# Performance work log

Hardware: AMD Instinct MI355X
Metric: run time of the kernel (lower is better)

## Reference

```python
import jax, jax.numpy as jnp
import numpy as np

N_NODES = 100000
N_HIDDEN = 128
N_EDGES = 625000
EPS = 1e-12  # F.normalize default eps


def setup_inputs() -> dict:
    key = jax.random.key(0)
    k1, k2, k3 = jax.random.split(key, 3)
    emb = jax.random.normal(k1, (N_NODES, N_HIDDEN), dtype=jnp.float32)
    edge_src = jax.random.randint(k2, (N_EDGES,), 0, N_NODES, dtype=jnp.int64)
    edge_dst = jax.random.randint(k3, (N_EDGES,), 0, N_NODES, dtype=jnp.int64)
    d = jnp.ones((N_HIDDEN,), dtype=jnp.float32)
    scale = jnp.ones((1,), dtype=jnp.float32)
    return {"emb": emb, "edge_src": edge_src, "edge_dst": edge_dst, "d": d, "scale": scale}


def reference(emb, edge_src, edge_dst, d, scale):
    # L2 normalize rows (torch F.normalize: x / max(||x||, eps))
    norm = jnp.linalg.norm(emb, axis=1, keepdims=True)
    e = emb / jnp.maximum(norm, EPS)            # [N, H]
    ew = e * d                                  # diag scale, [N, H]
    # edge-wise u_dot_v: sum over feature dim of ew[src] * e[dst]
    z = jnp.sum(ew[edge_src] * e[edge_dst], axis=1, keepdims=True)  # [E, 1]
    return z * scale
```

## Files before the change

kernel.cpp:

```cpp
#include <hip/hip_runtime.h>

#define NORM_EPS 1e-12f

#if defined(__has_builtin) && __has_builtin(__builtin_amdgcn_sdot4)
__device__ __forceinline__ int sdot4(unsigned a, unsigned b, int c) {
    return __builtin_amdgcn_sdot4((int)a, (int)b, c, false);
}
#else
__device__ __forceinline__ int sdot4(unsigned a, unsigned b, int c) {
    #pragma unroll
    for (int i = 0; i < 4; ++i)
        c += (int)(signed char)(a >> (8 * i)) * (int)(signed char)(b >> (8 * i));
    return c;
}
#endif

__global__ void build_tables_kernel(const float* __restrict__ emb,
                                    const float* __restrict__ dvec,
                                    unsigned short* __restrict__ tblW,
                                    unsigned short* __restrict__ tblE,
                                    float* __restrict__ sclW,
                                    float* __restrict__ sclE,
                                    int n_nodes) {
    int row  = (blockIdx.x * blockDim.x + threadIdx.x) >> 6;
    int lane = threadIdx.x & 63;
    if (row >= n_nodes) return;

    const float2* p = (const float2*)(emb + (size_t)row * 128);
    float2 v = p[lane];
    float s = v.x * v.x + v.y * v.y;
    #pragma unroll
    for (int off = 32; off > 0; off >>= 1)
        s += __shfl_xor(s, off);
    float inv = 1.0f / fmaxf(sqrtf(s), NORM_EPS);

    float e0 = v.x * inv, e1 = v.y * inv;
    float2 d2 = ((const float2*)dvec)[lane];
    float w0 = e0 * d2.x, w1 = e1 * d2.y;

    float mW = fmaxf(fabsf(w0), fabsf(w1));
    float mE = fmaxf(fabsf(e0), fabsf(e1));
    #pragma unroll
    for (int off = 32; off > 0; off >>= 1) {
        mW = fmaxf(mW, __shfl_xor(mW, off));
        mE = fmaxf(mE, __shfl_xor(mE, off));
    }

    float qW = (mW > 0.f) ? 127.0f / mW : 0.f;
    float qE = (mE > 0.f) ? 127.0f / mE : 0.f;
    int qw0 = __float2int_rn(w0 * qW), qw1 = __float2int_rn(w1 * qW);
    int qe0 = __float2int_rn(e0 * qE), qe1 = __float2int_rn(e1 * qE);

    tblW[(size_t)row * 64 + lane] =
        (unsigned short)((qw0 & 0xFF) | ((qw1 & 0xFF) << 8));
    tblE[(size_t)row * 64 + lane] =
        (unsigned short)((qe0 & 0xFF) | ((qe1 & 0xFF) << 8));
    if (lane == 0) {
        sclW[row] = mW * (1.0f / 127.0f);
        sclE[row] = mE * (1.0f / 127.0f);
    }
}

__global__ void edge_dot_i8_kernel(const uint4* __restrict__ tW,
                                   const uint4* __restrict__ tE,
                                   const float* __restrict__ sW,
                                   const float* __restrict__ sE,
                                   const int* __restrict__ esrc,
                                   const int* __restrict__ edst,
                                   const float* __restrict__ scale,
                                   float* __restrict__ out,
                                   int n_edges) {
    int g    = (blockIdx.x * blockDim.x + threadIdx.x) >> 3;
    int lane = threadIdx.x & 7;
    int e0 = g * 2, e1 = e0 + 1;
    if (e0 >= n_edges) return;
    bool has1 = e1 < n_edges;

    int s0 = esrc[e0], t0 = edst[e0];
    int s1 = has1 ? esrc[e1] : s0;
    int t1 = has1 ? edst[e1] : t0;

    uint4 a0 = tW[(size_t)s0 * 8 + lane];
    uint4 b0 = tE[(size_t)t0 * 8 + lane];
    uint4 a1 = tW[(size_t)s1 * 8 + lane];
    uint4 b1 = tE[(size_t)t1 * 8 + lane];

    float ss0 = sW[s0] * sE[t0];
    float ss1 = sW[s1] * sE[t1];

    int i0 = 0, i1 = 0;
    i0 = sdot4(a0.x, b0.x, i0); i0 = sdot4(a0.y, b0.y, i0);
    i0 = sdot4(a0.z, b0.z, i0); i0 = sdot4(a0.w, b0.w, i0);
    i1 = sdot4(a1.x, b1.x, i1); i1 = sdot4(a1.y, b1.y, i1);
    i1 = sdot4(a1.z, b1.z, i1); i1 = sdot4(a1.w, b1.w, i1);

    #pragma unroll
    for (int off = 4; off > 0; off >>= 1) {
        i0 += __shfl_xor(i0, off);
        i1 += __shfl_xor(i1, off);
    }

    if (lane == 0) {
        float sc = scale[0];
        out[e0] = (float)i0 * ss0 * sc;
        if (has1) out[e1] = (float)i1 * ss1 * sc;
    }
}

extern "C" void kernel_launch(void* const* d_in, const int* in_sizes, int n_in,
                              void* d_out, int out_size, void* d_ws, size_t ws_size,
                              hipStream_t stream) {
    const float* emb   = (const float*)d_in[0];
    const int*   esrc  = (const int*)d_in[1];
    const int*   edst  = (const int*)d_in[2];
    const float* dvec  = (const float*)d_in[3];
    const float* scale = (const float*)d_in[4];
    float*       out   = (float*)d_out;

    int n_nodes = in_sizes[0] / 128;
    int n_edges = in_sizes[1];

    char* base = (char*)d_ws;
    size_t tbl_bytes = (size_t)n_nodes * 128;
    unsigned short* tblW = (unsigned short*)base;
    unsigned short* tblE = (unsigned short*)(base + tbl_bytes);
    float*          sclW = (float*)(base + 2 * tbl_bytes);
    float*          sclE = (float*)(base + 2 * tbl_bytes + (size_t)n_nodes * 4);

    {
        int blocks = (n_nodes + 3) / 4;
        build_tables_kernel<<<blocks, 256, 0, stream>>>(
            emb, dvec, tblW, tblE, sclW, sclE, n_nodes);
    }
    {
        int n_groups = (n_edges + 1) / 2;
        long long threads = (long long)n_groups * 8;
        int blocks = (int)((threads + 255) / 256);
        edge_dot_i8_kernel<<<blocks, 256, 0, stream>>>(
            (const uint4*)tblW, (const uint4*)tblE, sclW, sclE,
            esrc, edst, scale, out, n_edges);
    }
}
```

Baseline: 131.5 us.

## Fold diagonal scale symmetrically via sqrt(|d|) to share one int8 table

Splits the diagonal weight as sqrt(|d|) on both sides of the dot product, so a single quantized table and a single scale array serve both source and destination gathers when d has no negative entries. A second sign-flipped table is written only when d contains negatives, chosen at runtime through a flag. This halves the table footprint in the common case, which should improve L2/MALL hit rates for the random gathers and cut build-kernel writes. The cost is an extra flag read per thread and slightly different quantization error.

```diff
diff --git a/kernel.cpp b/kernel.cpp
--- a/kernel.cpp
+++ b/kernel.cpp
@@ -17,10 +17,10 @@
 
 __global__ void build_tables_kernel(const float* __restrict__ emb,
                                     const float* __restrict__ dvec,
+                                    unsigned short* __restrict__ tblE,
                                     unsigned short* __restrict__ tblW,
-                                    unsigned short* __restrict__ tblE,
-                                    float* __restrict__ sclW,
-                                    float* __restrict__ sclE,
+                                    float* __restrict__ scl,
+                                    int* __restrict__ flag,
                                     int n_nodes) {
     int row  = (blockIdx.x * blockDim.x + threadIdx.x) >> 6;
     int lane = threadIdx.x & 63;
@@ -34,37 +34,40 @@
         s += __shfl_xor(s, off);
     float inv = 1.0f / fmaxf(sqrtf(s), NORM_EPS);
 
-    float e0 = v.x * inv, e1 = v.y * inv;
     float2 d2 = ((const float2*)dvec)[lane];
-    float w0 = e0 * d2.x, w1 = e1 * d2.y;
+    bool neg_lane = (d2.x < 0.0f) || (d2.y < 0.0f);
+    int has_neg = (__ballot(neg_lane) != 0ull) ? 1 : 0;
 
-    float mW = fmaxf(fabsf(w0), fabsf(w1));
-    float mE = fmaxf(fabsf(e0), fabsf(e1));
+    float r0 = sqrtf(fabsf(d2.x)), r1 = sqrtf(fabsf(d2.y));
+    float e0 = v.x * inv * r0, e1 = v.y * inv * r1;
+
+    float m = fmaxf(fabsf(e0), fabsf(e1));
     #pragma unroll
-    for (int off = 32; off > 0; off >>= 1) {
-        mW = fmaxf(mW, __shfl_xor(mW, off));
-        mE = fmaxf(mE, __shfl_xor(mE, off));
-    }
+    for (int off = 32; off > 0; off >>= 1)
+        m = fmaxf(m, __shfl_xor(m, off));
 
-    float qW = (mW > 0.f) ? 127.0f / mW : 0.f;
-    float qE = (mE > 0.f) ? 127.0f / mE : 0.f;
-    int qw0 = __float2int_rn(w0 * qW), qw1 = __float2int_rn(w1 * qW);
-    int qe0 = __float2int_rn(e0 * qE), qe1 = __float2int_rn(e1 * qE);
-
-    tblW[(size_t)row * 64 + lane] =
-        (unsigned short)((qw0 & 0xFF) | ((qw1 & 0xFF) << 8));
+    float q = (m > 0.f) ? 127.0f / m : 0.f;
+    int qe0 = __float2int_rn(e0 * q), qe1 = __float2int_rn(e1 * q);
     tblE[(size_t)row * 64 + lane] =
         (unsigned short)((qe0 & 0xFF) | ((qe1 & 0xFF) << 8));
+
+    if (has_neg) {
+        float w0 = (d2.x < 0.0f) ? -e0 : e0;
+        float w1 = (d2.y < 0.0f) ? -e1 : e1;
+        int qw0 = __float2int_rn(w0 * q), qw1 = __float2int_rn(w1 * q);
+        tblW[(size_t)row * 64 + lane] =
+            (unsigned short)((qw0 & 0xFF) | ((qw1 & 0xFF) << 8));
+    }
     if (lane == 0) {
-        sclW[row] = mW * (1.0f / 127.0f);
-        sclE[row] = mE * (1.0f / 127.0f);
+        scl[row] = m * (1.0f / 127.0f);
+        if (row == 0) flag[0] = has_neg;
     }
 }
 
-__global__ void edge_dot_i8_kernel(const uint4* __restrict__ tW,
-                                   const uint4* __restrict__ tE,
-                                   const float* __restrict__ sW,
-                                   const float* __restrict__ sE,
+__global__ void edge_dot_i8_kernel(const uint4* __restrict__ tE,
+                                   const uint4* __restrict__ tW,
+                                   const float* __restrict__ scl,
+                                   const int* __restrict__ flag,
                                    const int* __restrict__ esrc,
                                    const int* __restrict__ edst,
                                    const float* __restrict__ scale,
@@ -76,17 +79,19 @@
     if (e0 >= n_edges) return;
     bool has1 = e1 < n_edges;
 
+    const uint4* tS = (flag[0] != 0) ? tW : tE;
+
     int s0 = esrc[e0], t0 = edst[e0];
     int s1 = has1 ? esrc[e1] : s0;
     int t1 = has1 ? edst[e1] : t0;
 
-    uint4 a0 = tW[(size_t)s0 * 8 + lane];
+    uint4 a0 = tS[(size_t)s0 * 8 + lane];
     uint4 b0 = tE[(size_t)t0 * 8 + lane];
-    uint4 a1 = tW[(size_t)s1 * 8 + lane];
+    uint4 a1 = tS[(size_t)s1 * 8 + lane];
     uint4 b1 = tE[(size_t)t1 * 8 + lane];
 
-    float ss0 = sW[s0] * sE[t0];
-    float ss1 = sW[s1] * sE[t1];
+    float ss0 = scl[s0] * scl[t0];
+    float ss1 = scl[s1] * scl[t1];
 
     int i0 = 0, i1 = 0;
     i0 = sdot4(a0.x, b0.x, i0); i0 = sdot4(a0.y, b0.y, i0);
@@ -122,22 +127,22 @@
 
     char* base = (char*)d_ws;
     size_t tbl_bytes = (size_t)n_nodes * 128;
-    unsigned short* tblW = (unsigned short*)base;
-    unsigned short* tblE = (unsigned short*)(base + tbl_bytes);
-    float*          sclW = (float*)(base + 2 * tbl_bytes);
-    float*          sclE = (float*)(base + 2 * tbl_bytes + (size_t)n_nodes * 4);
+    unsigned short* tblE = (unsigned short*)base;
+    unsigned short* tblW = (unsigned short*)(base + tbl_bytes);
+    float*          scl  = (float*)(base + 2 * tbl_bytes);
+    int*            flag = (int*)(base + 2 * tbl_bytes + (size_t)n_nodes * 4);
 
     {
         int blocks = (n_nodes + 3) / 4;
         build_tables_kernel<<<blocks, 256, 0, stream>>>(
-            emb, dvec, tblW, tblE, sclW, sclE, n_nodes);
+            emb, dvec, tblE, tblW, scl, flag, n_nodes);
     }
     {
         int n_groups = (n_edges + 1) / 2;
         long long threads = (long long)n_groups * 8;
         int blocks = (int)((threads + 255) / 256);
         edge_dot_i8_kernel<<<blocks, 256, 0, stream>>>(
-            (const uint4*)tblW, (const uint4*)tblE, sclW, sclE,
+            (const uint4*)tblE, (const uint4*)tblW, scl, flag,
             esrc, edst, scale, out, n_edges);
     }
 }
```

Result: faster. 124.7 us (-5.2%).
